# Performance work log

Hardware: AMD Instinct MI355X
Metric: run time of the kernel (lower is better)

## Reference

```python
import jax, jax.numpy as jnp
import numpy as np

# dims
B, Nt, Ln, Lv = 16, 64, 256, 4      # batch, trees/batch, nodes/tree, value tokens/node
D = 256                              # embedding_dim
VOCAB, NTYPE = 32000, 64
M, Ls = 128, 4                       # story memory slots, tokens per slot
HOPS = 3                             # max_hops
COMP_STEP = 4                        # max tree depth = max(kb_n_layers)
LEVELS = [0, 1, 16, 64, 160, Ln]     # node index ranges per depth 0..4


def setup_inputs() -> dict:
    rng = np.random.default_rng(0)
    key = jax.random.key(0)
    ks = jax.random.split(key, 12)

    # --- tree structure: depth per node, father index in previous level ---
    depth = np.zeros(Ln, np.int64)
    father = np.zeros((B, Nt, Ln), np.int64)
    for lvl in range(1, 5):
        lo, hi = LEVELS[lvl], LEVELS[lvl + 1]
        depth[lo:hi] = lvl
        father[..., lo:hi] = rng.integers(LEVELS[lvl - 1], LEVELS[lvl], (B, Nt, hi - lo))
    father[..., 0] = Ln  # root's father = pad slot (torch -1 wraps to last index)
    kb_fathers = np.concatenate([father, np.full((B, Nt, 1), Ln, np.int64)], -1)  # [B,Nt,Ln+1]
    nl = np.broadcast_to(depth, (B, Nt, Ln))
    kb_n_layers = np.concatenate([nl, np.full((B, Nt, 1), -1, np.int64)], -1)     # [B,Nt,Ln+1]

    kb_values = rng.integers(1, VOCAB, (B, Nt, Ln, Lv))
    kb_types = rng.integers(1, NTYPE, (B, Nt, Ln))
    story = rng.integers(1, VOCAB, (B, M, Ls))
    decoder_input = rng.integers(1, VOCAB, (B,))

    s = 1.0 / np.sqrt(D)
    C = 0.1 * jax.random.normal(ks[0], (HOPS + 1, VOCAB, D), jnp.float32)
    C = C.at[:, 0].set(0.0)  # padding_idx = 0
    T_emb = 0.1 * jax.random.normal(ks[1], (NTYPE, D), jnp.float32)
    T_emb = T_emb.at[0].set(0.0)
    return {
        'decoder_input': jnp.asarray(decoder_input),
        'story': jnp.asarray(story),
        'hidden': 0.1 * jax.random.normal(ks[2], (1, B, D), jnp.float32),
        'kb_values': jnp.asarray(kb_values),
        'kb_types': jnp.asarray(kb_types),
        'kb_fathers': jnp.asarray(kb_fathers),
        'kb_n_layers': jnp.asarray(kb_n_layers),
        'C': C,
        'T_emb': T_emb,
        'Wq': s * jax.random.normal(ks[3], (D, D), jnp.float32),
        'Wk': s * jax.random.normal(ks[4], (D, D), jnp.float32),
        'Wv': s * jax.random.normal(ks[5], (D, D), jnp.float32),
        'W1_w': s * jax.random.normal(ks[6], (VOCAB, 2 * D), jnp.float32),
        'W1_b': jnp.zeros((VOCAB,), jnp.float32),
        'W_ih': s * jax.random.normal(ks[7], (3 * D, D), jnp.float32),
        'W_hh': s * jax.random.normal(ks[8], (3 * D, D), jnp.float32),
        'b_ih': jnp.zeros((3 * D,), jnp.float32),
        'b_hh': jnp.zeros((3 * D,), jnp.float32),
    }


def _forward(decoder_input, story, hidden, kb_values, kb_types, kb_fathers, kb_n_layers,
             C, T_emb, Wq, Wk, Wv, W1_w, W1_b, W_ih, W_hh, b_ih, b_hh):
    C0 = C[0]
    # ensemble: node embed = type_embed * sum(value token embeds)   [B,Nt,Ln,D]
    node = T_emb[kb_types] * C0[kb_values].sum(-2)
    node = jnp.concatenate([node, jnp.zeros((B, Nt, 1, D), node.dtype)], axis=2)  # pad slot
    nl = COMP_STEP - 1 - kb_n_layers  # adjusted layer counter
    base = jnp.arange(B * Nt).reshape(B, Nt, 1) * (Ln + 1)
    seg = (base + kb_fathers).reshape(-1)  # flat father ids for scatter-add

    def body(i, carry):
        node, nl = carry
        nxt = jax.ops.segment_sum(node.reshape(-1, D), seg,
                                  num_segments=B * Nt * (Ln + 1)).reshape(B, Nt, Ln + 1, D)
        node = node + nxt * (nl == 0)[..., None].astype(node.dtype)
        return (node, nl - 1)

    node, _ = jax.lax.fori_loop(0, COMP_STEP, body, (node, nl))
    roots = node[:, :, 0]                                   # [B,Nt,D]
    bias = jnp.where(roots.sum(-1) == 0, -1e9, 0.0)         # attention_bias [B,Nt]

    # compute_global_ranking: QKV attention over tree roots
    h = hidden[-1]                                          # [B,D]
    w = jax.nn.softmax(jnp.einsum('bnd,bd->bn', roots @ Wk.T, h @ Wq.T) + bias, axis=1)
    feat = jnp.einsum('bn,bnd->bd', w, roots @ Wv.T)        # kb_attn_features

    # single GRU step (PyTorch gate order r,z,n)
    x = C0[decoder_input]
    gi = x @ W_ih.T + b_ih
    gh = h @ W_hh.T + b_hh
    ir, iz, inn = jnp.split(gi, 3, -1)
    hr, hz, hn = jnp.split(gh, 3, -1)
    r = jax.nn.sigmoid(ir + hr)
    z = jax.nn.sigmoid(iz + hz)
    n = jnp.tanh(inn + r * hn)
    h_new = (1.0 - z) * n + z * h
    u = h_new + feat                                        # cur_state

    # ptrMemDecoder (Mem2Seq-style hops over story memory)
    p_vocab = None
    logits = None
    for hop in range(HOPS):
        m_A = C[hop][story].sum(2)                          # [B,M,D]
        logits = jnp.einsum('bmd,bd->bm', m_A, u)
        prob = jax.nn.softmax(logits, axis=1)
        m_C = C[hop + 1][story].sum(2)
        o = jnp.einsum('bm,bmd->bd', prob, m_C)
        if hop == 0:
            p_vocab = jnp.concatenate([u, o], -1) @ W1_w.T + W1_b
        u = u + o
    p_ptr = logits
    return p_ptr, p_vocab, h_new


def reference(decoder_input, story, hidden, kb_values, kb_types, kb_fathers, kb_n_layers,
              C, T_emb, Wq, Wk, Wv, W1_w, W1_b, W_ih, W_hh, b_ih, b_hh):
    return _forward(decoder_input, story, hidden, kb_values, kb_types, kb_fathers, kb_n_layers,
                    C, T_emb, Wq, Wk, Wv, W1_w, W1_b, W_ih, W_hh, b_ih, b_hh)
```

## Files before the change

kernel.cpp:

```cpp
#include <hip/hip_runtime.h>
#include <hip/hip_bf16.h>
#include <math.h>

#define B_ 16
#define NT 64
#define LN 256
#define LV 4
#define D_ 256
#define VOCAB_ 32000
#define M_ 128
#define LS 4
#define ECAP 352

typedef unsigned short ushort_t;
typedef unsigned int uint_t;

__device__ __forceinline__ ushort_t f2bf(float f) {
  uint_t u = __float_as_uint(f);
  uint_t r = u + 0x7FFFu + ((u >> 16) & 1u);
  return (ushort_t)(r >> 16);
}
__device__ __forceinline__ float bflo(uint_t u) {
  return __uint_as_float(u << 16);
}
__device__ __forceinline__ float bfhi(uint_t u) {
  return __uint_as_float(u & 0xFFFF0000u);
}

#define NB_S (3 * B_ * M_)
#define NB_CONV 2048
#define NB_TR 192
#define NB_TQK 256
#define NB_WVT 64
#define NB_BKT (B_ * NT)
__global__ __launch_bounds__(256) void k_prep(
    const int* __restrict__ story, const float* __restrict__ C,
    const float* __restrict__ W_ih, const float* __restrict__ W_hh,
    const float* __restrict__ Wq, const float* __restrict__ Wk,
    const float* __restrict__ Wv, const int* __restrict__ kb_values,
    const int* __restrict__ kb_types, float* __restrict__ S,
    ushort_t* __restrict__ C0h, float* __restrict__ W_ihT,
    float* __restrict__ W_hhT, float* __restrict__ TQK,
    float* __restrict__ WvT, int* __restrict__ entries,
    int* __restrict__ counts, int* __restrict__ qctr) {
  __shared__ __align__(16) char praw[6400];
  float* smem = (float*)praw;
  int blk = blockIdx.x, tid = threadIdx.x;
  if (blk == 0 && tid < 8) qctr[tid] = 0;
  if (blk < NB_S) {
    int h = blk / (B_ * M_);
    int bm = blk % (B_ * M_);
    const int* st = story + (size_t)bm * LS;
    const float* Ch = C + (size_t)h * VOCAB_ * D_;
    float s = Ch[(size_t)st[0] * D_ + tid] + Ch[(size_t)st[1] * D_ + tid] +
              Ch[(size_t)st[2] * D_ + tid] + Ch[(size_t)st[3] * D_ + tid];
    S[(size_t)blk * D_ + tid] = s;
  } else if (blk < NB_S + NB_CONV) {
    int n4 = VOCAB_ * D_ / 4;
    for (int i = (blk - NB_S) * 256 + tid; i < n4; i += NB_CONV * 256) {
      float4 f = ((const float4*)C)[i];
      uint2 packed;
      packed.x = (uint_t)f2bf(f.x) | ((uint_t)f2bf(f.y) << 16);
      packed.y = (uint_t)f2bf(f.z) | ((uint_t)f2bf(f.w) << 16);
      ((uint2*)C0h)[i] = packed;
    }
  } else if (blk < NB_S + NB_CONV + 2 * NB_TR) {
    int t = blk - (NB_S + NB_CONV);
    const float* W = W_ih;
    float* WT = W_ihT;
    if (t >= NB_TR) { t -= NB_TR; W = W_hh; WT = W_hhT; }
    const int R = 768;
    int tr = t % (R / 32), tc = t / (R / 32);
    int tx = tid & 31, ty = tid >> 5;
#pragma unroll
    for (int k = 0; k < 4; ++k)
      smem[(ty + 8 * k) * 33 + tx] =
          W[(size_t)(tr * 32 + ty + 8 * k) * D_ + tc * 32 + tx];
    __syncthreads();
#pragma unroll
    for (int k = 0; k < 4; ++k)
      WT[(size_t)(tc * 32 + ty + 8 * k) * R + tr * 32 + tx] =
          smem[tx * 33 + ty + 8 * k];
  } else if (blk < NB_S + NB_CONV + 2 * NB_TR + NB_TQK) {
    int j = blk - (NB_S + NB_CONV + 2 * NB_TR);
    smem[tid] = Wq[(size_t)tid * D_ + j];
    __syncthreads();
    float acc = 0.f;
#pragma unroll 8
    for (int k = 0; k < D_; ++k) acc += smem[k] * Wk[(size_t)k * D_ + tid];
    TQK[(size_t)j * D_ + tid] = acc;
  } else if (blk < NB_S + NB_CONV + 2 * NB_TR + NB_TQK + NB_WVT) {
    int t = blk - (NB_S + NB_CONV + 2 * NB_TR + NB_TQK);
    int tr = t & 7, tc = t >> 3;
    int tx = tid & 31, ty = tid >> 5;
#pragma unroll
    for (int k = 0; k < 4; ++k)
      smem[(ty + 8 * k) * 33 + tx] =
          Wv[(size_t)(tr * 32 + ty + 8 * k) * D_ + tc * 32 + tx];
    __syncthreads();
#pragma unroll
    for (int k = 0; k < 4; ++k)
      WvT[(size_t)(tc * 32 + ty + 8 * k) * D_ + tr * 32 + tx] =
          smem[tx * 33 + ty + 8 * k];
  } else {
    int bn = blk - (NB_S + NB_CONV + 2 * NB_TR + NB_TQK + NB_WVT);
    int* sval = (int*)praw;
    int* stype = sval + 1024;
    int* sbin = stype + 256;
    int* srng = sbin + 256;
    const int* vp = kb_values + (size_t)bn * LN * LV;
    for (int i = tid; i < LN * LV; i += 256) sval[i] = vp[i];
    stype[tid] = kb_types[(size_t)bn * LN + tid];
    sbin[tid] = 0;
    __syncthreads();
    int ty = stype[tid];
    int vv[4];
#pragma unroll
    for (int j = 0; j < 4; ++j) {
      vv[j] = sval[tid * 4 + j];
      atomicAdd(&sbin[((vv[j] >> 13) << 6) | ty], 1);
    }
    __syncthreads();
    if (tid < 64) {
      int run = 0;
#pragma unroll
      for (int c = 0; c < 4; ++c) {
        int x = sbin[c * 64 + tid];
        int orig = x;
        for (int o = 1; o < 64; o <<= 1) {
          int y = __shfl_up(x, o);
          if ((int)tid >= o) x += y;
        }
        sbin[c * 64 + tid] = x - orig + run;
        run += __shfl(x, 63);
      }
    }
    __syncthreads();
    if (tid < 4) {
      srng[tid] = sbin[tid << 6];
      int e = (tid == 3) ? (LN * LV) : sbin[(tid + 1) << 6];
      counts[bn * 4 + tid] = min(e - sbin[tid << 6], ECAP);
    }
    __syncthreads();
#pragma unroll
    for (int j = 0; j < 4; ++j) {
      int v = vv[j];
      int r = v >> 13;
      int pos = atomicAdd(&sbin[(r << 6) | ty], 1) - srng[r];
      if (pos < ECAP)
        entries[(size_t)(bn * 4 + r) * ECAP + pos] = v | (ty << 16);
    }
  }
}

#define NBG 512
#define UNITS_PER_RANGE 128
__global__ __launch_bounds__(512) void k_rootsg(
    const int* __restrict__ counts, const int* __restrict__ entries,
    const ushort_t* __restrict__ C0h, const float* __restrict__ T_emb,
    const int* __restrict__ dec, const float* __restrict__ C0,
    const float* __restrict__ hidden, const float* __restrict__ W_ihT,
    const float* __restrict__ W_hhT, const float* __restrict__ TQK,
    const float* __restrict__ b_ih, const float* __restrict__ b_hh,
    float* __restrict__ part, float* __restrict__ gi, float* __restrict__ gh,
    float* __restrict__ tvec, int* __restrict__ qctr) {
  __shared__ __align__(16) char smem_raw[64512 + 11264 + 16];
  int blk = blockIdx.x, tid = threadIdx.x;
  if (blk < NBG) {
    float4* t4s = (float4*)smem_raw;
    int* ent_all = (int*)(smem_raw + 64512);
    int* sunit = (int*)(smem_raw + 64512 + 11264);
    const float4* Tg = (const float4*)(T_emb + D_);
    for (int i = tid; i < 63 * 64; i += 512) t4s[i] = Tg[i];
    if (tid == 0) {
      int xcd = __builtin_amdgcn_s_getreg(6164) & 7;
      int r0 = xcd >> 1;
      int unit = -1;
      for (int a = 0; a < 4 && unit < 0; ++a) {
        int rr = (r0 + a) & 3;
        int u = atomicAdd(&qctr[rr], 1);
        if (u < UNITS_PER_RANGE) unit = (u << 2) | rr;
      }
      sunit[0] = unit;
    }
    __syncthreads();
    int unit = sunit[0];
    if (unit < 0) return;
    int rr = unit & 3, u = unit >> 2;
    int wid = tid >> 6, lane = tid & 63;
    int bn = u * 8 + wid;
    int bucket = bn * 4 + rr;
    int cnt = counts[bucket];
    const int* ge = entries + (size_t)bucket * ECAP;
    int* ent = ent_all + wid * ECAP;
    for (int i = lane; i < cnt; i += 64) ent[i] = ge[i];
    float a0 = 0.f, a1 = 0.f, a2 = 0.f, a3 = 0.f;
    int k = 0;
#pragma unroll 2
    for (; k + 4 <= cnt; k += 4) {
      int4 e4 = *(const int4*)(ent + k);
      int ex = __builtin_amdgcn_readfirstlane(e4.x);
      int ey = __builtin_amdgcn_readfirstlane(e4.y);
      int ez = __builtin_amdgcn_readfirstlane(e4.z);
      int ew = __builtin_amdgcn_readfirstlane(e4.w);
      uint2 u0 = ((const uint2*)(C0h + ((size_t)(ex & 0xFFFF) << 8)))[lane];
      uint2 u1 = ((const uint2*)(C0h + ((size_t)(ey & 0xFFFF) << 8)))[lane];
      uint2 u2 = ((const uint2*)(C0h + ((size_t)(ez & 0xFFFF) << 8)))[lane];
      uint2 u3 = ((const uint2*)(C0h + ((size_t)(ew & 0xFFFF) << 8)))[lane];
      float4 t0 = t4s[((ex >> 16) - 1) * 64 + lane];
      float4 t1 = t4s[((ey >> 16) - 1) * 64 + lane];
      float4 t2 = t4s[((ez >> 16) - 1) * 64 + lane];
      float4 t3 = t4s[((ew >> 16) - 1) * 64 + lane];
      a0 += t0.x * bflo(u0.x) + t1.x * bflo(u1.x) + t2.x * bflo(u2.x) +
            t3.x * bflo(u3.x);
      a1 += t0.y * bfhi(u0.x) + t1.y * bfhi(u1.x) + t2.y * bfhi(u2.x) +
            t3.y * bfhi(u3.x);
      a2 += t0.z * bflo(u0.y) + t1.z * bflo(u1.y) + t2.z * bflo(u2.y) +
            t3.z * bflo(u3.y);
      a3 += t0.w * bfhi(u0.y) + t1.w * bfhi(u1.y) + t2.w * bfhi(u2.y) +
            t3.w * bfhi(u3.y);
    }
    for (; k < cnt; ++k) {
      int e = ent[k];
      int es = __builtin_amdgcn_readfirstlane(e);
      uint2 uu = ((const uint2*)(C0h + ((size_t)(es & 0xFFFF) << 8)))[lane];
      float4 t = t4s[((es >> 16) - 1) * 64 + lane];
      a0 += t.x * bflo(uu.x);
      a1 += t.y * bfhi(uu.x);
      a2 += t.z * bflo(uu.y);
      a3 += t.w * bfhi(uu.y);
    }
    float4 res;
    res.x = a0; res.y = a1; res.z = a2; res.w = a3;
    ((float4*)(part + (size_t)bucket * D_))[lane] = res;
  } else {
    int g = blk - NBG;
    float* xs = (float*)smem_raw;
    float acc[B_];
    int i = (g < 3 ? g : g - 3) * 256 + tid;
    if (g < 3) {
      float bias = (tid < 256) ? b_ih[i] : 0.f;
#pragma unroll
      for (int b = 0; b < B_; ++b) acc[b] = bias;
      for (int c = 0; c < 4; ++c) {
        __syncthreads();
        for (int idx = tid; idx < B_ * 64; idx += 512) {
          int b = idx >> 6, jj = idx & 63;
          xs[idx] = C0[(size_t)dec[b] * D_ + c * 64 + jj];
        }
        __syncthreads();
        if (tid < 256) {
#pragma unroll 4
          for (int jj = 0; jj < 64; ++jj) {
            float w = W_ihT[(size_t)(c * 64 + jj) * 768 + i];
#pragma unroll
            for (int b = 0; b < B_; ++b) acc[b] += xs[b * 64 + jj] * w;
          }
        }
      }
      if (tid < 256) {
#pragma unroll
        for (int b = 0; b < B_; ++b) gi[(size_t)b * 768 + i] = acc[b];
      }
    } else if (g < 6) {
      float bias = (tid < 256) ? b_hh[i] : 0.f;
#pragma unroll
      for (int b = 0; b < B_; ++b) acc[b] = bias;
      for (int c = 0; c < 4; ++c) {
        __syncthreads();
        for (int idx = tid; idx < B_ * 64; idx += 512) {
          int b = idx >> 6, jj = idx & 63;
          xs[idx] = hidden[b * D_ + c * 64 + jj];
        }
        __syncthreads();
        if (tid < 256) {
#pragma unroll 4
          for (int jj = 0; jj < 64; ++jj) {
            float w = W_hhT[(size_t)(c * 64 + jj) * 768 + i];
#pragma unroll
            for (int b = 0; b < B_; ++b) acc[b] += xs[b * 64 + jj] * w;
          }
        }
      }
      if (tid < 256) {
#pragma unroll
        for (int b = 0; b < B_; ++b) gh[(size_t)b * 768 + i] = acc[b];
      }
    } else {
#pragma unroll
      for (int b = 0; b < B_; ++b) acc[b] = 0.f;
      for (int c = 0; c < 4; ++c) {
        __syncthreads();
        for (int idx = tid; idx < B_ * 64; idx += 512) {
          int b = idx >> 6, jj = idx & 63;
          xs[idx] = hidden[b * D_ + c * 64 + jj];
        }
        __syncthreads();
        if (tid < 256) {
#pragma unroll 4
          for (int jj = 0; jj < 64; ++jj) {
            float w = TQK[(size_t)(c * 64 + jj) * D_ + tid];
#pragma unroll
            for (int b = 0; b < B_; ++b) acc[b] += xs[b * 64 + jj] * w;
          }
        }
      }
      if (tid < 256) {
#pragma unroll
        for (int b = 0; b < B_; ++b) tvec[b * D_ + tid] = acc[b];
      }
    }
  }
}

__global__ __launch_bounds__(256) void k_mid(
    const float* __restrict__ part, const float* __restrict__ tvec,
    const float* __restrict__ S, float* __restrict__ scores,
    float* __restrict__ ST, float* __restrict__ rsum) {
  int blk = blockIdx.x, tid = threadIdx.x;
  if (blk < 1024) {
    int b = blk >> 6;
    const float* p = part + (size_t)blk * 4 * D_;
    float rv = p[tid] + p[D_ + tid] + p[2 * D_ + tid] + p[3 * D_ + tid];
    rsum[(size_t)blk * D_ + tid] = rv;
    float sc = rv * tvec[b * D_ + tid];
    float sm = rv;
    __shared__ float red[8];
    int lane = tid & 63, wave = tid >> 6;
    for (int o = 32; o > 0; o >>= 1) {
      sc += __shfl_xor(sc, o);
      sm += __shfl_xor(sm, o);
    }
    if (lane == 0) { red[wave] = sc; red[4 + wave] = sm; }
    __syncthreads();
    if (tid == 0) {
      float SC = red[0] + red[1] + red[2] + red[3];
      float SM = red[4] + red[5] + red[6] + red[7];
      scores[blk] = (SM == 0.0f) ? SC - 1000000000.0f : SC;
    }
  } else {
    int t = blk - 1024;
    int hb = t >> 5;
    int tile = t & 31;
    int tm = tile & 3, td = tile >> 2;
    int tx = tid & 31, ty = tid >> 5;
    __shared__ float sm2[32 * 33];
    const float* Sp = S + (size_t)hb * M_ * D_;
    float* STp = ST + (size_t)hb * D_ * M_;
#pragma unroll
    for (int k = 0; k < 4; ++k)
      sm2[(ty + 8 * k) * 33 + tx] =
          Sp[(size_t)(tm * 32 + ty + 8 * k) * D_ + td * 32 + tx];
    __syncthreads();
#pragma unroll
    for (int k = 0; k < 4; ++k)
      STp[(size_t)(td * 32 + ty + 8 * k) * M_ + tm * 32 + tx] =
          sm2[tx * 33 + ty + 8 * k];
  }
}

__global__ __launch_bounds__(256) void k_chain(
    const float* __restrict__ scores, const float* __restrict__ rsum,
    const float* __restrict__ WvT, const float* __restrict__ gi,
    const float* __restrict__ gh, const float* __restrict__ hidden,
    const float* __restrict__ S, const float* __restrict__ ST,
    float* __restrict__ h_new_out, float* __restrict__ cat,
    float* __restrict__ p_ptr) {
  int b = blockIdx.x, tid = threadIdx.x;
  __shared__ float wsh[NT], rs[D_], us[D_], lo[M_], loB[M_], pr[M_];
  if (tid < NT) {
    float s = scores[b * NT + tid];
    float m = s;
    for (int o = 32; o > 0; o >>= 1) m = fmaxf(m, __shfl_xor(m, o));
    float e = expf(s - m);
    float sum = e;
    for (int o = 32; o > 0; o >>= 1) sum += __shfl_xor(sum, o);
    wsh[tid] = e / sum;
  }
  __syncthreads();
  float rb = 0.f;
#pragma unroll 16
  for (int n = 0; n < NT; ++n)
    rb += wsh[n] * rsum[(size_t)(b * NT + n) * D_ + tid];
  rs[tid] = rb;
  __syncthreads();
  float feat = 0.f;
#pragma unroll 16
  for (int j = 0; j < D_; ++j) feat += rs[j] * WvT[(size_t)j * D_ + tid];
  {
    float i_r = gi[(size_t)b * 768 + tid];
    float i_z = gi[(size_t)b * 768 + 256 + tid];
    float i_n = gi[(size_t)b * 768 + 512 + tid];
    float h_r = gh[(size_t)b * 768 + tid];
    float h_z = gh[(size_t)b * 768 + 256 + tid];
    float h_n = gh[(size_t)b * 768 + 512 + tid];
    float h = hidden[b * D_ + tid];
    float r = 1.f / (1.f + expf(-(i_r + h_r)));
    float z = 1.f / (1.f + expf(-(i_z + h_z)));
    float nn = tanhf(i_n + r * h_n);
    float hn = (1.f - z) * nn + z * h;
    h_new_out[b * D_ + tid] = hn;
    float u0 = hn + feat;
    us[tid] = u0;
    cat[b * 512 + tid] = u0;
  }
  __syncthreads();
  for (int h = 0; h < 3; ++h) {
    {
      int m = tid & 127;
      int half = tid >> 7;
      const float* STp = ST + (((size_t)h * B_ + b) * D_ + half * 128) * M_;
      float l = 0.f;
#pragma unroll 16
      for (int d = 0; d < 128; ++d)
        l += us[half * 128 + d] * STp[(size_t)d * M_ + m];
      if (half == 0) lo[m] = l; else loB[m] = l;
    }
    __syncthreads();
    if (h == 2) {
      if (tid < M_) p_ptr[b * M_ + tid] = lo[tid] + loB[tid];
      break;
    }
    if (tid < 64) {
      float l0 = lo[tid] + loB[tid], l1 = lo[tid + 64] + loB[tid + 64];
      float a = fmaxf(l0, l1);
      for (int o = 32; o > 0; o >>= 1) a = fmaxf(a, __shfl_xor(a, o));
      float e0 = expf(l0 - a), e1 = expf(l1 - a);
      float s = e0 + e1;
      for (int o = 32; o > 0; o >>= 1) s += __shfl_xor(s, o);
      pr[tid] = e0 / s;
      pr[tid + 64] = e1 / s;
    }
    __syncthreads();
    {
      const float* Sn = S + (((size_t)(h + 1) * B_ + b) * M_) * D_;
      float o = 0.f;
#pragma unroll 16
      for (int m = 0; m < M_; ++m) o += pr[m] * Sn[(size_t)m * D_ + tid];
      if (h == 0) cat[b * 512 + D_ + tid] = o;
      us[tid] += o;
    }
    __syncthreads();
  }
}

__global__ __launch_bounds__(256) void k_pvocab(
    const float* __restrict__ cat, const float* __restrict__ W1_w,
    const float* __restrict__ W1_b, float* __restrict__ out) {
  int blk = blockIdx.x, tid = threadIdx.x;
  int row = tid & 63, q = tid >> 6;
  int v = blk * 64 + row;
  __shared__ float cs[B_ * 512];
  __shared__ float ps[3][64][B_];
  for (int i = tid; i < B_ * 512; i += 256) cs[i] = cat[i];
  __syncthreads();
  const float4* wrow = (const float4*)(W1_w + (size_t)v * 512 + q * 128);
  float acc[B_];
#pragma unroll
  for (int b = 0; b < B_; ++b) acc[b] = 0.f;
#pragma unroll 4
  for (int k4 = 0; k4 < 32; ++k4) {
    float4 w = wrow[k4];
#pragma unroll
    for (int b = 0; b < B_; ++b) {
      const float* c = &cs[b * 512 + q * 128 + k4 * 4];
      acc[b] += w.x * c[0] + w.y * c[1] + w.z * c[2] + w.w * c[3];
    }
  }
  if (q > 0) {
#pragma unroll
    for (int b = 0; b < B_; ++b) ps[q - 1][row][b] = acc[b];
  }
  __syncthreads();
  if (q == 0) {
    float bb = W1_b[v];
#pragma unroll
    for (int b = 0; b < B_; ++b)
      out[(size_t)b * VOCAB_ + v] =
          acc[b] + ps[0][row][b] + ps[1][row][b] + ps[2][row][b] + bb;
  }
}

extern "C" void kernel_launch(void* const* d_in, const int* in_sizes, int n_in,
                              void* d_out, int out_size, void* d_ws,
                              size_t ws_size, hipStream_t stream) {
  const int* decoder_input = (const int*)d_in[0];
  const int* story = (const int*)d_in[1];
  const float* hidden = (const float*)d_in[2];
  const int* kb_values = (const int*)d_in[3];
  const int* kb_types = (const int*)d_in[4];
  const float* C = (const float*)d_in[7];
  const float* T_emb = (const float*)d_in[8];
  const float* Wq = (const float*)d_in[9];
  const float* Wk = (const float*)d_in[10];
  const float* Wv = (const float*)d_in[11];
  const float* W1_w = (const float*)d_in[12];
  const float* W1_b = (const float*)d_in[13];
  const float* W_ih = (const float*)d_in[14];
  const float* W_hh = (const float*)d_in[15];
  const float* b_ih = (const float*)d_in[16];
  const float* b_hh = (const float*)d_in[17];

  float* out = (float*)d_out;
  float* p_ptr = out;
  float* p_vocab = out + B_ * M_;
  float* h_new = out + B_ * M_ + B_ * VOCAB_;

  float* ws = (float*)d_ws;
  float* S = ws;
  float* part = S + 3 * B_ * M_ * D_;
  float* rsum = part + B_ * NT * 4 * D_;
  float* cat = rsum + B_ * NT * D_;
  float* scores = cat + B_ * 512;
  float* gi = scores + B_ * NT;
  float* gh = gi + B_ * 768;
  float* tvec = gh + B_ * 768;
  int* counts = (int*)(tvec + B_ * D_);
  int* qctr = counts + 4096;
  ushort_t* C0h = (ushort_t*)(qctr + 8);
  float* wtmp = (float*)(C0h + (size_t)VOCAB_ * D_);
  float* W_ihT = wtmp;
  float* W_hhT = W_ihT + 768 * D_;
  float* TQK = W_hhT + 768 * D_;
  int* entries = (int*)(TQK + D_ * D_);
  float* ST = wtmp;
  float* WvT = wtmp + (458752 + 1441792);

  hipLaunchKernelGGL(
      k_prep, dim3(NB_S + NB_CONV + 2 * NB_TR + NB_TQK + NB_WVT + NB_BKT),
      dim3(256), 0, stream, story, C, W_ih, W_hh, Wq, Wk, Wv, kb_values,
      kb_types, S, C0h, W_ihT, W_hhT, TQK, WvT, entries, counts, qctr);
  hipLaunchKernelGGL(k_rootsg, dim3(NBG + 7), dim3(512), 0, stream, counts,
                     entries, C0h, T_emb, decoder_input, C, hidden, W_ihT,
                     W_hhT, TQK, b_ih, b_hh, part, gi, gh, tvec, qctr);
  hipLaunchKernelGGL(k_mid, dim3(1024 + 1536), dim3(256), 0, stream, part,
                     tvec, S, scores, ST, rsum);
  hipLaunchKernelGGL(k_chain, dim3(B_), dim3(256), 0, stream, scores, rsum,
                     WvT, gi, gh, hidden, S, ST, h_new, cat, p_ptr);
  hipLaunchKernelGGL(k_pvocab, dim3(VOCAB_ / 64), dim3(256), 0, stream, cat,
                     W1_w, W1_b, p_vocab);
}
```

Measured before the change: 381.2 us.

## Restructure root gather into half-wave 16-byte loads over zero-padded entry lists

The gather block in k_rootsg now uses 1024 threads covering 16 buckets. Each half-wave processes one entry, loading 16 bytes of the bf16 embedding row per lane, and the two halves are combined with a cross-half shuffle at the end. Entry lists are zero-padded to a multiple of 8 in k_prep. This removes the tail loop and the LDS staging of entries, because padding entries point at the zero embedding row and the zero type row. The aim is more memory-level parallelism and wider loads, at the cost of a larger block, tight launch bounds, and more idle threads in the GEMV blocks, which use only 256 of the 1024 threads.

```diff
diff --git a/kernel.cpp b/kernel.cpp
--- a/kernel.cpp
+++ b/kernel.cpp
@@ -108,6 +108,7 @@
     int* stype = sval + 1024;
     int* sbin = stype + 256;
     int* srng = sbin + 256;
+    int* scnt = srng + 4;
     const int* vp = kb_values + (size_t)bn * LN * LV;
     for (int i = tid; i < LN * LV; i += 256) sval[i] = vp[i];
     stype[tid] = kb_types[(size_t)bn * LN + tid];
@@ -139,7 +140,9 @@
     if (tid < 4) {
       srng[tid] = sbin[tid << 6];
       int e = (tid == 3) ? (LN * LV) : sbin[(tid + 1) << 6];
-      counts[bn * 4 + tid] = min(e - sbin[tid << 6], ECAP);
+      int cv = min(e - sbin[tid << 6], ECAP);
+      counts[bn * 4 + tid] = cv;
+      scnt[tid] = cv;
     }
     __syncthreads();
 #pragma unroll
@@ -150,12 +153,19 @@
       if (pos < ECAP)
         entries[(size_t)(bn * 4 + r) * ECAP + pos] = v | (ty << 16);
     }
-  }
-}
-
-#define NBG 512
-#define UNITS_PER_RANGE 128
-__global__ __launch_bounds__(512) void k_rootsg(
+    __syncthreads();
+    if (tid < 4) {
+      int cv = scnt[tid];
+      int cp = (cv + 7) & ~7;
+      for (int p = cv; p < cp; ++p)
+        entries[(size_t)(bn * 4 + tid) * ECAP + p] = 0;
+    }
+  }
+}
+
+#define NBG 256
+#define UNITS_PER_RANGE 64
+__global__ __launch_bounds__(1024, 8) void k_rootsg(
     const int* __restrict__ counts, const int* __restrict__ entries,
     const ushort_t* __restrict__ C0h, const float* __restrict__ T_emb,
     const int* __restrict__ dec, const float* __restrict__ C0,
@@ -164,14 +174,13 @@
     const float* __restrict__ b_ih, const float* __restrict__ b_hh,
     float* __restrict__ part, float* __restrict__ gi, float* __restrict__ gh,
     float* __restrict__ tvec, int* __restrict__ qctr) {
-  __shared__ __align__(16) char smem_raw[64512 + 11264 + 16];
+  __shared__ __align__(16) char smem_raw[65552];
   int blk = blockIdx.x, tid = threadIdx.x;
   if (blk < NBG) {
     float4* t4s = (float4*)smem_raw;
-    int* ent_all = (int*)(smem_raw + 64512);
-    int* sunit = (int*)(smem_raw + 64512 + 11264);
-    const float4* Tg = (const float4*)(T_emb + D_);
-    for (int i = tid; i < 63 * 64; i += 512) t4s[i] = Tg[i];
+    int* sunit = (int*)(smem_raw + 65536);
+    const float4* Tg = (const float4*)T_emb;
+    for (int i = tid; i < 64 * 64; i += 1024) t4s[i] = Tg[i];
     if (tid == 0) {
       int xcd = __builtin_amdgcn_s_getreg(6164) & 7;
       int r0 = xcd >> 1;
@@ -184,55 +193,54 @@
       sunit[0] = unit;
     }
     __syncthreads();
-    int unit = sunit[0];
+    int unit = __builtin_amdgcn_readfirstlane(sunit[0]);
     if (unit < 0) return;
     int rr = unit & 3, u = unit >> 2;
-    int wid = tid >> 6, lane = tid & 63;
-    int bn = u * 8 + wid;
+    int wid = __builtin_amdgcn_readfirstlane(tid >> 6);
+    int lane = tid & 63;
+    int l31 = lane & 31;
+    int half = lane >> 5;
+    int bn = u * 16 + wid;
     int bucket = bn * 4 + rr;
     int cnt = counts[bucket];
+    int cntp = (cnt + 7) & ~7;
     const int* ge = entries + (size_t)bucket * ECAP;
-    int* ent = ent_all + wid * ECAP;
-    for (int i = lane; i < cnt; i += 64) ent[i] = ge[i];
     float a0 = 0.f, a1 = 0.f, a2 = 0.f, a3 = 0.f;
-    int k = 0;
-#pragma unroll 2
-    for (; k + 4 <= cnt; k += 4) {
-      int4 e4 = *(const int4*)(ent + k);
-      int ex = __builtin_amdgcn_readfirstlane(e4.x);
-      int ey = __builtin_amdgcn_readfirstlane(e4.y);
-      int ez = __builtin_amdgcn_readfirstlane(e4.z);
-      int ew = __builtin_amdgcn_readfirstlane(e4.w);
-      uint2 u0 = ((const uint2*)(C0h + ((size_t)(ex & 0xFFFF) << 8)))[lane];
-      uint2 u1 = ((const uint2*)(C0h + ((size_t)(ey & 0xFFFF) << 8)))[lane];
-      uint2 u2 = ((const uint2*)(C0h + ((size_t)(ez & 0xFFFF) << 8)))[lane];
-      uint2 u3 = ((const uint2*)(C0h + ((size_t)(ew & 0xFFFF) << 8)))[lane];
-      float4 t0 = t4s[((ex >> 16) - 1) * 64 + lane];
-      float4 t1 = t4s[((ey >> 16) - 1) * 64 + lane];
-      float4 t2 = t4s[((ez >> 16) - 1) * 64 + lane];
-      float4 t3 = t4s[((ew >> 16) - 1) * 64 + lane];
-      a0 += t0.x * bflo(u0.x) + t1.x * bflo(u1.x) + t2.x * bflo(u2.x) +
-            t3.x * bflo(u3.x);
-      a1 += t0.y * bfhi(u0.x) + t1.y * bfhi(u1.x) + t2.y * bfhi(u2.x) +
-            t3.y * bfhi(u3.x);
-      a2 += t0.z * bflo(u0.y) + t1.z * bflo(u1.y) + t2.z * bflo(u2.y) +
-            t3.z * bflo(u3.y);
-      a3 += t0.w * bfhi(u0.y) + t1.w * bfhi(u1.y) + t2.w * bfhi(u2.y) +
-            t3.w * bfhi(u3.y);
-    }
-    for (; k < cnt; ++k) {
-      int e = ent[k];
-      int es = __builtin_amdgcn_readfirstlane(e);
-      uint2 uu = ((const uint2*)(C0h + ((size_t)(es & 0xFFFF) << 8)))[lane];
-      float4 t = t4s[((es >> 16) - 1) * 64 + lane];
-      a0 += t.x * bflo(uu.x);
-      a1 += t.y * bfhi(uu.x);
-      a2 += t.z * bflo(uu.y);
-      a3 += t.w * bfhi(uu.y);
-    }
-    float4 res;
-    res.x = a0; res.y = a1; res.z = a2; res.w = a3;
-    ((float4*)(part + (size_t)bucket * D_))[lane] = res;
+    float a4 = 0.f, a5 = 0.f, a6 = 0.f, a7 = 0.f;
+#pragma unroll 4
+    for (int k = 0; k < cntp; k += 2) {
+      int e0 = ge[k];
+      int e1 = ge[k + 1];
+      int e = half ? e1 : e0;
+      uint4 uu = ((const uint4*)(C0h + ((size_t)(e & 0xFFFF) << 8)))[l31];
+      int ty = e >> 16;
+      float4 ta = t4s[ty * 64 + 2 * l31];
+      float4 tb = t4s[ty * 64 + 2 * l31 + 1];
+      a0 += ta.x * bflo(uu.x);
+      a1 += ta.y * bfhi(uu.x);
+      a2 += ta.z * bflo(uu.y);
+      a3 += ta.w * bfhi(uu.y);
+      a4 += tb.x * bflo(uu.z);
+      a5 += tb.y * bfhi(uu.z);
+      a6 += tb.z * bflo(uu.w);
+      a7 += tb.w * bfhi(uu.w);
+    }
+    a0 += __shfl_xor(a0, 32);
+    a1 += __shfl_xor(a1, 32);
+    a2 += __shfl_xor(a2, 32);
+    a3 += __shfl_xor(a3, 32);
+    a4 += __shfl_xor(a4, 32);
+    a5 += __shfl_xor(a5, 32);
+    a6 += __shfl_xor(a6, 32);
+    a7 += __shfl_xor(a7, 32);
+    if (half == 0) {
+      float4 r0v, r1v;
+      r0v.x = a0; r0v.y = a1; r0v.z = a2; r0v.w = a3;
+      r1v.x = a4; r1v.y = a5; r1v.z = a6; r1v.w = a7;
+      float4* pp = (float4*)(part + (size_t)bucket * D_ + 8 * l31);
+      pp[0] = r0v;
+      pp[1] = r1v;
+    }
   } else {
     int g = blk - NBG;
     float* xs = (float*)smem_raw;
@@ -244,7 +252,7 @@
       for (int b = 0; b < B_; ++b) acc[b] = bias;
       for (int c = 0; c < 4; ++c) {
         __syncthreads();
-        for (int idx = tid; idx < B_ * 64; idx += 512) {
+        for (int idx = tid; idx < B_ * 64; idx += 1024) {
           int b = idx >> 6, jj = idx & 63;
           xs[idx] = C0[(size_t)dec[b] * D_ + c * 64 + jj];
         }
@@ -268,7 +276,7 @@
       for (int b = 0; b < B_; ++b) acc[b] = bias;
       for (int c = 0; c < 4; ++c) {
         __syncthreads();
-        for (int idx = tid; idx < B_ * 64; idx += 512) {
+        for (int idx = tid; idx < B_ * 64; idx += 1024) {
           int b = idx >> 6, jj = idx & 63;
           xs[idx] = hidden[b * D_ + c * 64 + jj];
         }
@@ -291,7 +299,7 @@
       for (int b = 0; b < B_; ++b) acc[b] = 0.f;
       for (int c = 0; c < 4; ++c) {
         __syncthreads();
-        for (int idx = tid; idx < B_ * 64; idx += 512) {
+        for (int idx = tid; idx < B_ * 64; idx += 1024) {
           int b = idx >> 6, jj = idx & 63;
           xs[idx] = hidden[b * D_ + c * 64 + jj];
         }
@@ -530,7 +538,7 @@
       k_prep, dim3(NB_S + NB_CONV + 2 * NB_TR + NB_TQK + NB_WVT + NB_BKT),
       dim3(256), 0, stream, story, C, W_ih, W_hh, Wq, Wk, Wv, kb_values,
       kb_types, S, C0h, W_ihT, W_hhT, TQK, WvT, entries, counts, qctr);
-  hipLaunchKernelGGL(k_rootsg, dim3(NBG + 7), dim3(512), 0, stream, counts,
+  hipLaunchKernelGGL(k_rootsg, dim3(NBG + 7), dim3(1024), 0, stream, counts,
                      entries, C0h, T_emb, decoder_input, C, hidden, W_ihT,
                      W_hhT, TQK, b_ih, b_hh, part, gi, gh, tvec, qctr);
   hipLaunchKernelGGL(k_mid, dim3(1024 + 1536), dim3(256), 0, stream, part,
```

Measured after the change: 512.9 us. +34.5%, slower.

## Split root gather into 8 vocab ranges and half-D tiles for cache locality

Applied to the files above, without the earlier changes.

Tree-value entries are now bucketed into 8 vocab ranges instead of 4, and each gather unit handles only half of the embedding dimension. This doubles the range count and splits each unit across two D-halves, so the bf16 table working set per XCD shrinks and the T_emb shared-memory tile halves, allowing more resident blocks (launch_bounds 512,8). Entry lists are zero-padded to a multiple of 8 so the scalar tail loop is dropped, and k_mid now sums 8 partials instead of 4. The cost is more blocks and more partial buffers. The smaller ECAP of 192 risks truncating buckets whose counts exceed it.

```diff
diff --git a/kernel.cpp b/kernel.cpp
--- a/kernel.cpp
+++ b/kernel.cpp
@@ -10,7 +10,7 @@
 #define VOCAB_ 32000
 #define M_ 128
 #define LS 4
-#define ECAP 352
+#define ECAP 192
 
 typedef unsigned short ushort_t;
 typedef unsigned int uint_t;
@@ -43,7 +43,7 @@
     float* __restrict__ W_hhT, float* __restrict__ TQK,
     float* __restrict__ WvT, int* __restrict__ entries,
     int* __restrict__ counts, int* __restrict__ qctr) {
-  __shared__ __align__(16) char praw[6400];
+  __shared__ __align__(16) char praw[7424];
   float* smem = (float*)praw;
   int blk = blockIdx.x, tid = threadIdx.x;
   if (blk == 0 && tid < 8) qctr[tid] = 0;
@@ -107,24 +107,26 @@
     int* sval = (int*)praw;
     int* stype = sval + 1024;
     int* sbin = stype + 256;
-    int* srng = sbin + 256;
+    int* srng = sbin + 512;
+    int* scnt = srng + 8;
     const int* vp = kb_values + (size_t)bn * LN * LV;
     for (int i = tid; i < LN * LV; i += 256) sval[i] = vp[i];
     stype[tid] = kb_types[(size_t)bn * LN + tid];
     sbin[tid] = 0;
+    sbin[256 + tid] = 0;
     __syncthreads();
     int ty = stype[tid];
     int vv[4];
 #pragma unroll
     for (int j = 0; j < 4; ++j) {
       vv[j] = sval[tid * 4 + j];
-      atomicAdd(&sbin[((vv[j] >> 13) << 6) | ty], 1);
+      atomicAdd(&sbin[((vv[j] >> 12) << 6) | ty], 1);
     }
     __syncthreads();
     if (tid < 64) {
       int run = 0;
 #pragma unroll
-      for (int c = 0; c < 4; ++c) {
+      for (int c = 0; c < 8; ++c) {
         int x = sbin[c * 64 + tid];
         int orig = x;
         for (int o = 1; o < 64; o <<= 1) {
@@ -136,26 +138,36 @@
       }
     }
     __syncthreads();
-    if (tid < 4) {
+    if (tid < 8) {
       srng[tid] = sbin[tid << 6];
-      int e = (tid == 3) ? (LN * LV) : sbin[(tid + 1) << 6];
-      counts[bn * 4 + tid] = min(e - sbin[tid << 6], ECAP);
+      int e = (tid == 7) ? (LN * LV) : sbin[(tid + 1) << 6];
+      int cv = min(e - sbin[tid << 6], ECAP);
+      counts[bn * 8 + tid] = cv;
+      scnt[tid] = cv;
     }
     __syncthreads();
 #pragma unroll
     for (int j = 0; j < 4; ++j) {
       int v = vv[j];
-      int r = v >> 13;
+      int r = v >> 12;
       int pos = atomicAdd(&sbin[(r << 6) | ty], 1) - srng[r];
       if (pos < ECAP)
-        entries[(size_t)(bn * 4 + r) * ECAP + pos] = v | (ty << 16);
-    }
-  }
-}
-
-#define NBG 512
-#define UNITS_PER_RANGE 128
-__global__ __launch_bounds__(512) void k_rootsg(
+        entries[(size_t)(bn * 8 + r) * ECAP + pos] = v | (ty << 16);
+    }
+    __syncthreads();
+    if (tid < 8) {
+      int cv = scnt[tid];
+      int cp = (cv + 7) & ~7;
+      for (int p = cv; p < cp; ++p)
+        entries[(size_t)(bn * 8 + tid) * ECAP + p] = 0;
+    }
+  }
+}
+
+#define NBG 2048
+#define NRANGE 8
+#define UNITS_PER_RANGE 256
+__global__ __launch_bounds__(512, 8) void k_rootsg(
     const int* __restrict__ counts, const int* __restrict__ entries,
     const ushort_t* __restrict__ C0h, const float* __restrict__ T_emb,
     const int* __restrict__ dec, const float* __restrict__ C0,
@@ -164,75 +176,65 @@
     const float* __restrict__ b_ih, const float* __restrict__ b_hh,
     float* __restrict__ part, float* __restrict__ gi, float* __restrict__ gh,
     float* __restrict__ tvec, int* __restrict__ qctr) {
-  __shared__ __align__(16) char smem_raw[64512 + 11264 + 16];
+  __shared__ __align__(16) char smem_raw[32768 + 6144 + 16];
   int blk = blockIdx.x, tid = threadIdx.x;
   if (blk < NBG) {
-    float4* t4s = (float4*)smem_raw;
-    int* ent_all = (int*)(smem_raw + 64512);
-    int* sunit = (int*)(smem_raw + 64512 + 11264);
-    const float4* Tg = (const float4*)(T_emb + D_);
-    for (int i = tid; i < 63 * 64; i += 512) t4s[i] = Tg[i];
+    float2* t2s = (float2*)smem_raw;
+    int* ent_all = (int*)(smem_raw + 32768);
+    int* sunit = (int*)(smem_raw + 32768 + 6144);
     if (tid == 0) {
       int xcd = __builtin_amdgcn_s_getreg(6164) & 7;
-      int r0 = xcd >> 1;
       int unit = -1;
-      for (int a = 0; a < 4 && unit < 0; ++a) {
-        int rr = (r0 + a) & 3;
+      for (int a = 0; a < NRANGE && unit < 0; ++a) {
+        int rr = (xcd + a) & 7;
         int u = atomicAdd(&qctr[rr], 1);
-        if (u < UNITS_PER_RANGE) unit = (u << 2) | rr;
+        if (u < UNITS_PER_RANGE) unit = (u << 3) | rr;
       }
       sunit[0] = unit;
     }
     __syncthreads();
     int unit = sunit[0];
     if (unit < 0) return;
-    int rr = unit & 3, u = unit >> 2;
+    int rr = unit & 7, u = unit >> 3;
+    int h = u & 1, grp = u >> 1;
+    const float2* Tg = (const float2*)T_emb;
+    for (int i = tid; i < 64 * 64; i += 512)
+      t2s[i] = Tg[(i >> 6) * 128 + h * 64 + (i & 63)];
     int wid = tid >> 6, lane = tid & 63;
-    int bn = u * 8 + wid;
-    int bucket = bn * 4 + rr;
+    int bn = grp * 8 + wid;
+    int bucket = bn * 8 + rr;
     int cnt = counts[bucket];
+    int cntp = (cnt + 7) & ~7;
     const int* ge = entries + (size_t)bucket * ECAP;
     int* ent = ent_all + wid * ECAP;
-    for (int i = lane; i < cnt; i += 64) ent[i] = ge[i];
-    float a0 = 0.f, a1 = 0.f, a2 = 0.f, a3 = 0.f;
-    int k = 0;
+    for (int i = lane; i < cntp; i += 64) ent[i] = ge[i];
+    __syncthreads();
+    const ushort_t* C0hh = C0h + h * 128 + 2 * lane;
+    float a0 = 0.f, a1 = 0.f;
 #pragma unroll 2
-    for (; k + 4 <= cnt; k += 4) {
+    for (int k = 0; k < cntp; k += 4) {
       int4 e4 = *(const int4*)(ent + k);
       int ex = __builtin_amdgcn_readfirstlane(e4.x);
       int ey = __builtin_amdgcn_readfirstlane(e4.y);
       int ez = __builtin_amdgcn_readfirstlane(e4.z);
       int ew = __builtin_amdgcn_readfirstlane(e4.w);
-      uint2 u0 = ((const uint2*)(C0h + ((size_t)(ex & 0xFFFF) << 8)))[lane];
-      uint2 u1 = ((const uint2*)(C0h + ((size_t)(ey & 0xFFFF) << 8)))[lane];
-      uint2 u2 = ((const uint2*)(C0h + ((size_t)(ez & 0xFFFF) << 8)))[lane];
-      uint2 u3 = ((const uint2*)(C0h + ((size_t)(ew & 0xFFFF) << 8)))[lane];
-      float4 t0 = t4s[((ex >> 16) - 1) * 64 + lane];
-      float4 t1 = t4s[((ey >> 16) - 1) * 64 + lane];
-      float4 t2 = t4s[((ez >> 16) - 1) * 64 + lane];
-      float4 t3 = t4s[((ew >> 16) - 1) * 64 + lane];
-      a0 += t0.x * bflo(u0.x) + t1.x * bflo(u1.x) + t2.x * bflo(u2.x) +
-            t3.x * bflo(u3.x);
-      a1 += t0.y * bfhi(u0.x) + t1.y * bfhi(u1.x) + t2.y * bfhi(u2.x) +
-            t3.y * bfhi(u3.x);
-      a2 += t0.z * bflo(u0.y) + t1.z * bflo(u1.y) + t2.z * bflo(u2.y) +
-            t3.z * bflo(u3.y);
-      a3 += t0.w * bfhi(u0.y) + t1.w * bfhi(u1.y) + t2.w * bfhi(u2.y) +
-            t3.w * bfhi(u3.y);
-    }
-    for (; k < cnt; ++k) {
-      int e = ent[k];
-      int es = __builtin_amdgcn_readfirstlane(e);
-      uint2 uu = ((const uint2*)(C0h + ((size_t)(es & 0xFFFF) << 8)))[lane];
-      float4 t = t4s[((es >> 16) - 1) * 64 + lane];
-      a0 += t.x * bflo(uu.x);
-      a1 += t.y * bfhi(uu.x);
-      a2 += t.z * bflo(uu.y);
-      a3 += t.w * bfhi(uu.y);
-    }
-    float4 res;
-    res.x = a0; res.y = a1; res.z = a2; res.w = a3;
-    ((float4*)(part + (size_t)bucket * D_))[lane] = res;
+      uint_t u0 = *(const uint_t*)(C0hh + ((size_t)(ex & 0xFFFF) << 8));
+      uint_t u1 = *(const uint_t*)(C0hh + ((size_t)(ey & 0xFFFF) << 8));
+      uint_t u2 = *(const uint_t*)(C0hh + ((size_t)(ez & 0xFFFF) << 8));
+      uint_t u3 = *(const uint_t*)(C0hh + ((size_t)(ew & 0xFFFF) << 8));
+      float2 t0 = t2s[((ex >> 16) << 6) | lane];
+      float2 t1 = t2s[((ey >> 16) << 6) | lane];
+      float2 t2 = t2s[((ez >> 16) << 6) | lane];
+      float2 t3 = t2s[((ew >> 16) << 6) | lane];
+      a0 += t0.x * bflo(u0) + t1.x * bflo(u1) + t2.x * bflo(u2) +
+            t3.x * bflo(u3);
+      a1 += t0.y * bfhi(u0) + t1.y * bfhi(u1) + t2.y * bfhi(u2) +
+            t3.y * bfhi(u3);
+    }
+    float2 res;
+    res.x = a0;
+    res.y = a1;
+    ((float2*)(part + (size_t)bucket * D_ + h * 128))[lane] = res;
   } else {
     int g = blk - NBG;
     float* xs = (float*)smem_raw;
@@ -320,8 +322,10 @@
   int blk = blockIdx.x, tid = threadIdx.x;
   if (blk < 1024) {
     int b = blk >> 6;
-    const float* p = part + (size_t)blk * 4 * D_;
-    float rv = p[tid] + p[D_ + tid] + p[2 * D_ + tid] + p[3 * D_ + tid];
+    const float* p = part + (size_t)blk * 8 * D_;
+    float rv = 0.f;
+#pragma unroll
+    for (int r = 0; r < 8; ++r) rv += p[r * D_ + tid];
     rsum[(size_t)blk * D_ + tid] = rv;
     float sc = rv * tvec[b * D_ + tid];
     float sm = rv;
@@ -509,14 +513,14 @@
   float* ws = (float*)d_ws;
   float* S = ws;
   float* part = S + 3 * B_ * M_ * D_;
-  float* rsum = part + B_ * NT * 4 * D_;
+  float* rsum = part + B_ * NT * 8 * D_;
   float* cat = rsum + B_ * NT * D_;
   float* scores = cat + B_ * 512;
   float* gi = scores + B_ * NT;
   float* gh = gi + B_ * 768;
   float* tvec = gh + B_ * 768;
   int* counts = (int*)(tvec + B_ * D_);
-  int* qctr = counts + 4096;
+  int* qctr = counts + 8192;
   ushort_t* C0h = (ushort_t*)(qctr + 8);
   float* wtmp = (float*)(C0h + (size_t)VOCAB_ * D_);
   float* W_ihT = wtmp;
@@ -524,7 +528,7 @@
   float* TQK = W_hhT + 768 * D_;
   int* entries = (int*)(TQK + D_ * D_);
   float* ST = wtmp;
-  float* WvT = wtmp + (458752 + 1441792);
+  float* WvT = wtmp + (458752 + 1572864);
 
   hipLaunchKernelGGL(
       k_prep, dim3(NB_S + NB_CONV + 2 * NB_TR + NB_TQK + NB_WVT + NB_BKT),
```

After: 608.1 us. 59.5% more time.
